# Kernel tuning notes

Measured on AMD Instinct MI355X. Metric: run time of the kernel, lower is better.

## Reference

```python
import jax, jax.numpy as jnp
import numpy as np

NEG_INF = -9e15
ALPHA = 2.0  # LeakyReLU negative slope from init (alpha=2)


def setup_inputs() -> dict:
    key = jax.random.key(0)
    k1, k2, k3, k4 = jax.random.split(key, 4)
    B, N, Fin, Fout = 8, 2048, 256, 128
    x = jax.random.normal(k1, (B, N, Fin), dtype=jnp.float32)
    adj = jax.random.randint(k2, (B, N, N), 0, 2, dtype=jnp.int32)
    # xavier_uniform with gain=1.414
    def xavier(k, shape, gain=1.414):
        fan_in, fan_out = shape[0], shape[1]
        bound = gain * np.sqrt(6.0 / (fan_in + fan_out))
        return jax.random.uniform(k, shape, jnp.float32, -bound, bound)
    W = xavier(k3, (Fin, Fout))
    a = xavier(k4, (2 * Fout, 1))
    return {"x": x, "adj": adj, "W": W, "a": a}


def reference(x, adj, W, a):
    # Wh: [B, N, Fout]
    Wh = jnp.matmul(x, W)
    Fout = W.shape[1]
    a1 = a[:Fout, 0]   # [Fout]
    a2 = a[Fout:, 0]   # [Fout]
    f1 = jnp.einsum('bnf,f->bn', Wh, a1)  # [B, N]
    f2 = jnp.einsum('bnf,f->bn', Wh, a2)  # [B, N]
    e = f1[:, :, None] + f2[:, None, :]   # [B, N, N]
    e = jnp.where(e >= 0, e, ALPHA * e)   # leaky relu, slope 2
    e = jnp.where(adj > 0, e, NEG_INF)
    attention = jax.nn.softmax(e, axis=2)
    # dropout: eval mode (no-op)
    h_prime = jnp.matmul(attention, Wh)   # [B, N, Fout]
    # concat=True -> elu
    return jnp.where(h_prime > 0, h_prime, jnp.expm1(h_prime))
```

## Files before the change

### kernel.cpp

```cpp
#include <hip/hip_runtime.h>
#include <hip/hip_bf16.h>
#include <math.h>

#define NEGINF (-9000000000000000.0f)

constexpr int B_   = 8;
constexpr int N_   = 2048;
constexpr int FIN  = 256;
constexpr int FOUT = 128;
constexpr int TI   = 16;
constexpr int PPAD = 8;
constexpr int PROW = N_ + PPAD;
constexpr int WPAD = 8;
constexpr int WROW = FIN + WPAD;

typedef __attribute__((ext_vector_type(8))) short bf16x8;
typedef __attribute__((ext_vector_type(4))) float f32x4;

static __device__ __forceinline__ unsigned short f2bf(float f) {
    __hip_bfloat16 h = __float2bfloat16(f);
    return *reinterpret_cast<unsigned short*>(&h);
}
static __device__ __forceinline__ float bf2f(unsigned short u) {
    unsigned int v = ((unsigned int)u) << 16;
    return *reinterpret_cast<float*>(&v);
}

__global__ __launch_bounds__(256) void k0_wt(const float* __restrict__ W,
                                             unsigned short* __restrict__ Wt) {
    const int n = blockIdx.x;
    const int k = threadIdx.x;
    Wt[n * FIN + k] = f2bf(W[k * FOUT + n]);
}

__global__ __launch_bounds__(256) void k1_wh(const float* __restrict__ x,
                                             const unsigned short* __restrict__ Wt,
                                             unsigned short* __restrict__ WhT) {
    __shared__ unsigned short wt[FOUT * WROW];
    __shared__ unsigned short xs[64 * WROW];
    const int tid = threadIdx.x;
    const long r0 = (long)blockIdx.x * 64;

    {
        const int4* src = (const int4*)Wt;
        for (int i = tid; i < FOUT * FIN / 8; i += 256) {
            int row = i >> 5;
            int c   = i & 31;
            *(int4*)&wt[row * WROW + c * 8] = src[i];
        }
    }
    {
        const float4* xsrc = (const float4*)(x + r0 * FIN);
        for (int i = tid; i < 64 * FIN / 4; i += 256) {
            float4 v = xsrc[i];
            int row = i >> 6;
            int c   = i & 63;
            ushort4 u;
            u.x = f2bf(v.x); u.y = f2bf(v.y); u.z = f2bf(v.z); u.w = f2bf(v.w);
            *(ushort4*)&xs[row * WROW + c * 4] = u;
        }
    }
    __syncthreads();

    const int wave = tid >> 6, lane = tid & 63;
    const int quad = lane >> 4, l16 = lane & 15;

    f32x4 acc[2][4];
#pragma unroll
    for (int a = 0; a < 2; ++a)
#pragma unroll
        for (int b = 0; b < 4; ++b) acc[a][b] = {0.f, 0.f, 0.f, 0.f};

#pragma unroll
    for (int ks = 0; ks < FIN / 32; ++ks) {
        const int kof = ks * 32 + quad * 8;
        bf16x8 afr[2], bfr[4];
#pragma unroll
        for (int a = 0; a < 2; ++a) {
            const int d = (wave * 2 + a) * 16 + l16;
            afr[a] = *(const bf16x8*)&wt[d * WROW + kof];
        }
#pragma unroll
        for (int b = 0; b < 4; ++b) {
            const int r = b * 16 + l16;
            bfr[b] = *(const bf16x8*)&xs[r * WROW + kof];
        }
#pragma unroll
        for (int a = 0; a < 2; ++a)
#pragma unroll
            for (int b = 0; b < 4; ++b)
                acc[a][b] = __builtin_amdgcn_mfma_f32_16x16x32_bf16(
                    afr[a], bfr[b], acc[a][b], 0, 0, 0);
    }

    const long bb = r0 / N_;
    const long jb = r0 % N_;
    unsigned short* dst = WhT + bb * (long)FOUT * N_;
#pragma unroll
    for (int a = 0; a < 2; ++a)
#pragma unroll
        for (int b = 0; b < 4; ++b) {
            const long j = jb + b * 16 + l16;
#pragma unroll
            for (int r = 0; r < 4; ++r) {
                const int d = (wave * 2 + a) * 16 + quad * 4 + r;
                dst[(long)d * N_ + j] = f2bf(acc[a][b][r]);
            }
        }
}

__global__ __launch_bounds__(256) void k1b_f(const unsigned short* __restrict__ WhT,
                                             const float* __restrict__ a,
                                             float* __restrict__ f1,
                                             float* __restrict__ f2) {
    __shared__ float a1s[FOUT], a2s[FOUT];
    const int tid = threadIdx.x;
    if (tid < FOUT) { a1s[tid] = a[tid]; a2s[tid] = a[FOUT + tid]; }
    __syncthreads();
    const long jflat = (long)blockIdx.x * 256 + tid;
    const long b = jflat / N_, j = jflat % N_;
    const unsigned short* src = WhT + b * (long)FOUT * N_ + j;
    float s1 = 0.f, s2 = 0.f;
#pragma unroll
    for (int d = 0; d < FOUT; ++d) {
        float w = bf2f(src[(long)d * N_]);
        s1 += w * a1s[d];
        s2 += w * a2s[d];
    }
    f1[jflat] = s1;
    f2[jflat] = s2;
}

__global__ __launch_bounds__(256) void k2_attn(const int* __restrict__ adj,
                                               const unsigned short* __restrict__ WhT,
                                               const float* __restrict__ f1,
                                               const float* __restrict__ f2,
                                               float* __restrict__ out) {
    __shared__ unsigned short p[TI * PROW];
    __shared__ float rsum[TI];

    const int tid  = threadIdx.x;
    const int b    = blockIdx.x & 7;
    const int i0   = (blockIdx.x >> 3) * TI;
    const int wave = tid >> 6, lane = tid & 63;
    const int quad = lane >> 4, l16 = lane & 15;

    const float4* f2b4 = (const float4*)(f2 + (size_t)b * N_);

    for (int rr = 0; rr < 4; ++rr) {
        const int ti = wave * 4 + rr;
        const int i  = i0 + ti;
        const float f1i = f1[(size_t)b * N_ + i];
        const int4* arow4 = (const int4*)(adj + ((size_t)b * N_ + i) * (size_t)N_);

        int4   av[8];
        float4 fv[8];
#pragma unroll
        for (int it = 0; it < 8; ++it) {
            av[it] = arow4[lane + it * 64];
            fv[it] = f2b4[lane + it * 64];
        }
        float4 e[8];
        float m = NEGINF;
#pragma unroll
        for (int it = 0; it < 8; ++it) {
            const float4 t = fv[it];
            float e0 = f1i + t.x; e0 = (e0 >= 0.f) ? e0 : 2.f * e0; if (av[it].x <= 0) e0 = NEGINF;
            float e1 = f1i + t.y; e1 = (e1 >= 0.f) ? e1 : 2.f * e1; if (av[it].y <= 0) e1 = NEGINF;
            float e2 = f1i + t.z; e2 = (e2 >= 0.f) ? e2 : 2.f * e2; if (av[it].z <= 0) e2 = NEGINF;
            float e3 = f1i + t.w; e3 = (e3 >= 0.f) ? e3 : 2.f * e3; if (av[it].w <= 0) e3 = NEGINF;
            e[it] = make_float4(e0, e1, e2, e3);
            m = fmaxf(m, fmaxf(fmaxf(e0, e1), fmaxf(e2, e3)));
        }
#pragma unroll
        for (int o = 32; o; o >>= 1) m = fmaxf(m, __shfl_xor(m, o));

        float s = 0.f;
        unsigned short* pr = &p[ti * PROW];
#pragma unroll
        for (int it = 0; it < 8; ++it) {
            const float p0 = __expf(e[it].x - m);
            const float p1 = __expf(e[it].y - m);
            const float p2 = __expf(e[it].z - m);
            const float p3 = __expf(e[it].w - m);
            s += (p0 + p1) + (p2 + p3);
            ushort4 u;
            u.x = f2bf(p0); u.y = f2bf(p1); u.z = f2bf(p2); u.w = f2bf(p3);
            *(ushort4*)&pr[(lane + it * 64) * 4] = u;
        }
#pragma unroll
        for (int o = 32; o; o >>= 1) s += __shfl_xor(s, o);
        if (lane == 0) rsum[ti] = s;
    }
    __syncthreads();

    const int n0 = wave * 32;
    const unsigned short* whb = WhT + (size_t)b * FOUT * N_;
    const unsigned short* pA  = &p[l16 * PROW];
    const unsigned short* wB0 = whb + (size_t)(n0 + l16) * N_;
    const unsigned short* wB1 = whb + (size_t)(n0 + 16 + l16) * N_;

    f32x4 acc0 = {0.f, 0.f, 0.f, 0.f}, acc1 = {0.f, 0.f, 0.f, 0.f};
#pragma unroll 4
    for (int ks = 0; ks < N_ / 32; ++ks) {
        const int kof = ks * 32 + quad * 8;
        bf16x8 afr = *(const bf16x8*)&pA[kof];
        bf16x8 b0  = *(const bf16x8*)&wB0[kof];
        bf16x8 b1  = *(const bf16x8*)&wB1[kof];
        acc0 = __builtin_amdgcn_mfma_f32_16x16x32_bf16(afr, b0, acc0, 0, 0, 0);
        acc1 = __builtin_amdgcn_mfma_f32_16x16x32_bf16(afr, b1, acc1, 0, 0, 0);
    }

#pragma unroll
    for (int r = 0; r < 4; ++r) {
        const int m = quad * 4 + r;
        const float inv = 1.f / rsum[m];
        float v0 = acc0[r] * inv;
        float v1 = acc1[r] * inv;
        v0 = (v0 > 0.f) ? v0 : expm1f(v0);
        v1 = (v1 > 0.f) ? v1 : expm1f(v1);
        const size_t base = ((size_t)b * N_ + i0 + m) * FOUT + n0;
        out[base + l16]      = v0;
        out[base + 16 + l16] = v1;
    }
}

extern "C" void kernel_launch(void* const* d_in, const int* in_sizes, int n_in,
                              void* d_out, int out_size, void* d_ws, size_t ws_size,
                              hipStream_t stream) {
    const float* x   = (const float*)d_in[0];
    const int*   adj = (const int*)d_in[1];
    const float* W   = (const float*)d_in[2];
    const float* a   = (const float*)d_in[3];
    float* out = (float*)d_out;

    unsigned short* WhT = (unsigned short*)d_ws;
    unsigned short* Wt  = WhT + (size_t)B_ * FOUT * N_;
    float* f1 = (float*)(Wt + (size_t)FOUT * FIN);
    float* f2 = f1 + (size_t)B_ * N_;

    hipLaunchKernelGGL(k0_wt, dim3(FOUT), dim3(FIN), 0, stream, W, Wt);
    hipLaunchKernelGGL(k1_wh, dim3(B_ * N_ / 64), dim3(256), 0, stream,
                       x, Wt, WhT);
    hipLaunchKernelGGL(k1b_f, dim3(B_ * N_ / 256), dim3(256), 0, stream,
                       WhT, a, f1, f2);
    hipLaunchKernelGGL(k2_attn, dim3(B_ * N_ / TI), dim3(256), 0, stream,
                       adj, WhT, f1, f2, out);
}
```

Measured before the change: 282.7 us.

## Fuse f1/f2 projection into Wh GEMM and chunk attention with online softmax

The f1/f2 attention projections move into the epilogue of the Wh GEMM. This drops a separate kernel that re-read WhT with strided column access. The Wh GEMM now uses 32-row tiles and reads Wt directly from global memory instead of staging it in shared memory. The attention kernel processes adjacency in 512-column chunks with a running max/sum rescale, shrinking the P buffer in LDS from 16x2048 to 16x512 to improve occupancy. The cost is an extra barrier per chunk and interleaving softmax with MFMA in phases, rather than one long streaming pass.

```diff
diff --git a/kernel.cpp b/kernel.cpp
--- a/kernel.cpp
+++ b/kernel.cpp
@@ -8,11 +8,11 @@
 constexpr int N_   = 2048;
 constexpr int FIN  = 256;
 constexpr int FOUT = 128;
-constexpr int TI   = 16;
-constexpr int PPAD = 8;
-constexpr int PROW = N_ + PPAD;
-constexpr int WPAD = 8;
-constexpr int WROW = FIN + WPAD;
+
+constexpr int CH  = 512;
+constexpr int NCH = N_ / CH;
+constexpr int PR  = CH + 8;
+constexpr int XR  = FIN + 8;
 
 typedef __attribute__((ext_vector_type(8))) short bf16x8;
 typedef __attribute__((ext_vector_type(4))) float f32x4;
@@ -20,10 +20,6 @@
 static __device__ __forceinline__ unsigned short f2bf(float f) {
     __hip_bfloat16 h = __float2bfloat16(f);
     return *reinterpret_cast<unsigned short*>(&h);
-}
-static __device__ __forceinline__ float bf2f(unsigned short u) {
-    unsigned int v = ((unsigned int)u) << 16;
-    return *reinterpret_cast<float*>(&v);
 }
 
 __global__ __launch_bounds__(256) void k0_wt(const float* __restrict__ W,
@@ -33,31 +29,32 @@
     Wt[n * FIN + k] = f2bf(W[k * FOUT + n]);
 }
 
-__global__ __launch_bounds__(256) void k1_wh(const float* __restrict__ x,
+__global__ __launch_bounds__(256) void ka_wh(const float* __restrict__ x,
                                              const unsigned short* __restrict__ Wt,
-                                             unsigned short* __restrict__ WhT) {
-    __shared__ unsigned short wt[FOUT * WROW];
-    __shared__ unsigned short xs[64 * WROW];
+                                             const float* __restrict__ a,
+                                             unsigned short* __restrict__ WhT,
+                                             float* __restrict__ f1,
+                                             float* __restrict__ f2) {
+    __shared__ unsigned short xs[32 * XR];
+    __shared__ float as[2 * FOUT];
+    __shared__ float fred[2][4][32];
+
     const int tid = threadIdx.x;
-    const long r0 = (long)blockIdx.x * 64;
-
+    const int j0  = blockIdx.x * 32;
+    const int b   = j0 >> 11;
+    const int jb  = j0 & (N_ - 1);
+
+    if (tid < 2 * FOUT) as[tid] = a[tid];
     {
-        const int4* src = (const int4*)Wt;
-        for (int i = tid; i < FOUT * FIN / 8; i += 256) {
-            int row = i >> 5;
-            int c   = i & 31;
-            *(int4*)&wt[row * WROW + c * 8] = src[i];
-        }
-    }
-    {
-        const float4* xsrc = (const float4*)(x + r0 * FIN);
-        for (int i = tid; i < 64 * FIN / 4; i += 256) {
-            float4 v = xsrc[i];
-            int row = i >> 6;
-            int c   = i & 63;
+        const float4* xsrc = (const float4*)(x + (size_t)j0 * FIN);
+#pragma unroll
+        for (int t = 0; t < 8; ++t) {
+            const int idx = tid + t * 256;
+            float4 v = xsrc[idx];
+            const int row = idx >> 6, c4 = idx & 63;
             ushort4 u;
             u.x = f2bf(v.x); u.y = f2bf(v.y); u.z = f2bf(v.z); u.w = f2bf(v.w);
-            *(ushort4*)&xs[row * WROW + c * 4] = u;
+            *(ushort4*)&xs[row * XR + c4 * 4] = u;
         }
     }
     __syncthreads();
@@ -65,150 +62,165 @@
     const int wave = tid >> 6, lane = tid & 63;
     const int quad = lane >> 4, l16 = lane & 15;
 
-    f32x4 acc[2][4];
-#pragma unroll
-    for (int a = 0; a < 2; ++a)
-#pragma unroll
-        for (int b = 0; b < 4; ++b) acc[a][b] = {0.f, 0.f, 0.f, 0.f};
-
+    f32x4 acc[2][2];
+#pragma unroll
+    for (int aa = 0; aa < 2; ++aa)
+#pragma unroll
+        for (int nn = 0; nn < 2; ++nn) acc[aa][nn] = {0.f, 0.f, 0.f, 0.f};
+
+    const unsigned short* wtA0 = Wt + (size_t)(32 * wave + l16) * FIN;
+    const unsigned short* wtA1 = wtA0 + 16 * FIN;
 #pragma unroll
     for (int ks = 0; ks < FIN / 32; ++ks) {
         const int kof = ks * 32 + quad * 8;
-        bf16x8 afr[2], bfr[4];
-#pragma unroll
-        for (int a = 0; a < 2; ++a) {
-            const int d = (wave * 2 + a) * 16 + l16;
-            afr[a] = *(const bf16x8*)&wt[d * WROW + kof];
-        }
-#pragma unroll
-        for (int b = 0; b < 4; ++b) {
-            const int r = b * 16 + l16;
-            bfr[b] = *(const bf16x8*)&xs[r * WROW + kof];
-        }
-#pragma unroll
-        for (int a = 0; a < 2; ++a)
-#pragma unroll
-            for (int b = 0; b < 4; ++b)
-                acc[a][b] = __builtin_amdgcn_mfma_f32_16x16x32_bf16(
-                    afr[a], bfr[b], acc[a][b], 0, 0, 0);
-    }
-
-    const long bb = r0 / N_;
-    const long jb = r0 % N_;
-    unsigned short* dst = WhT + bb * (long)FOUT * N_;
-#pragma unroll
-    for (int a = 0; a < 2; ++a)
-#pragma unroll
-        for (int b = 0; b < 4; ++b) {
-            const long j = jb + b * 16 + l16;
+        bf16x8 af0 = *(const bf16x8*)&wtA0[kof];
+        bf16x8 af1 = *(const bf16x8*)&wtA1[kof];
+        bf16x8 bf0 = *(const bf16x8*)&xs[l16 * XR + kof];
+        bf16x8 bf1 = *(const bf16x8*)&xs[(16 + l16) * XR + kof];
+        acc[0][0] = __builtin_amdgcn_mfma_f32_16x16x32_bf16(af0, bf0, acc[0][0], 0, 0, 0);
+        acc[0][1] = __builtin_amdgcn_mfma_f32_16x16x32_bf16(af0, bf1, acc[0][1], 0, 0, 0);
+        acc[1][0] = __builtin_amdgcn_mfma_f32_16x16x32_bf16(af1, bf0, acc[1][0], 0, 0, 0);
+        acc[1][1] = __builtin_amdgcn_mfma_f32_16x16x32_bf16(af1, bf1, acc[1][1], 0, 0, 0);
+    }
+
+    unsigned short* dst = WhT + (size_t)b * FOUT * N_;
+    float pf[2][2] = {{0.f, 0.f}, {0.f, 0.f}};
+#pragma unroll
+    for (int aa = 0; aa < 2; ++aa)
+#pragma unroll
+        for (int nn = 0; nn < 2; ++nn)
 #pragma unroll
             for (int r = 0; r < 4; ++r) {
-                const int d = (wave * 2 + a) * 16 + quad * 4 + r;
-                dst[(long)d * N_ + j] = f2bf(acc[a][b][r]);
+                const int d = 32 * wave + 16 * aa + 4 * quad + r;
+                const int j = jb + 16 * nn + l16;
+                const float v = acc[aa][nn][r];
+                dst[(size_t)d * N_ + j] = f2bf(v);
+                pf[0][nn] += v * as[d];
+                pf[1][nn] += v * as[FOUT + d];
             }
-        }
-}
-
-__global__ __launch_bounds__(256) void k1b_f(const unsigned short* __restrict__ WhT,
-                                             const float* __restrict__ a,
-                                             float* __restrict__ f1,
-                                             float* __restrict__ f2) {
-    __shared__ float a1s[FOUT], a2s[FOUT];
-    const int tid = threadIdx.x;
-    if (tid < FOUT) { a1s[tid] = a[tid]; a2s[tid] = a[FOUT + tid]; }
+#pragma unroll
+    for (int ff = 0; ff < 2; ++ff)
+#pragma unroll
+        for (int nn = 0; nn < 2; ++nn) {
+            float v = pf[ff][nn];
+            v += __shfl_xor(v, 16);
+            v += __shfl_xor(v, 32);
+            pf[ff][nn] = v;
+        }
+    if (quad == 0) {
+#pragma unroll
+        for (int ff = 0; ff < 2; ++ff)
+#pragma unroll
+            for (int nn = 0; nn < 2; ++nn)
+                fred[ff][wave][nn * 16 + l16] = pf[ff][nn];
+    }
     __syncthreads();
-    const long jflat = (long)blockIdx.x * 256 + tid;
-    const long b = jflat / N_, j = jflat % N_;
-    const unsigned short* src = WhT + b * (long)FOUT * N_ + j;
-    float s1 = 0.f, s2 = 0.f;
-#pragma unroll
-    for (int d = 0; d < FOUT; ++d) {
-        float w = bf2f(src[(long)d * N_]);
-        s1 += w * a1s[d];
-        s2 += w * a2s[d];
-    }
-    f1[jflat] = s1;
-    f2[jflat] = s2;
-}
-
-__global__ __launch_bounds__(256) void k2_attn(const int* __restrict__ adj,
+    if (tid < 64) {
+        const int ff = tid >> 5, j32 = tid & 31;
+        const float s = fred[ff][0][j32] + fred[ff][1][j32] +
+                        fred[ff][2][j32] + fred[ff][3][j32];
+        (ff ? f2 : f1)[(size_t)b * N_ + jb + j32] = s;
+    }
+}
+
+__global__ __launch_bounds__(256) void kb_attn(const int* __restrict__ adj,
                                                const unsigned short* __restrict__ WhT,
                                                const float* __restrict__ f1,
                                                const float* __restrict__ f2,
                                                float* __restrict__ out) {
-    __shared__ unsigned short p[TI * PROW];
-    __shared__ float rsum[TI];
+    __shared__ unsigned short p[16 * PR];
+    __shared__ float alpha_s[16];
+    __shared__ float rsum[16];
 
     const int tid  = threadIdx.x;
     const int b    = blockIdx.x & 7;
-    const int i0   = (blockIdx.x >> 3) * TI;
+    const int i0   = (blockIdx.x >> 3) * 16;
     const int wave = tid >> 6, lane = tid & 63;
     const int quad = lane >> 4, l16 = lane & 15;
 
     const float4* f2b4 = (const float4*)(f2 + (size_t)b * N_);
 
-    for (int rr = 0; rr < 4; ++rr) {
-        const int ti = wave * 4 + rr;
-        const int i  = i0 + ti;
-        const float f1i = f1[(size_t)b * N_ + i];
-        const int4* arow4 = (const int4*)(adj + ((size_t)b * N_ + i) * (size_t)N_);
-
-        int4   av[8];
-        float4 fv[8];
-#pragma unroll
-        for (int it = 0; it < 8; ++it) {
-            av[it] = arow4[lane + it * 64];
-            fv[it] = f2b4[lane + it * 64];
-        }
-        float4 e[8];
-        float m = NEGINF;
-#pragma unroll
-        for (int it = 0; it < 8; ++it) {
-            const float4 t = fv[it];
-            float e0 = f1i + t.x; e0 = (e0 >= 0.f) ? e0 : 2.f * e0; if (av[it].x <= 0) e0 = NEGINF;
-            float e1 = f1i + t.y; e1 = (e1 >= 0.f) ? e1 : 2.f * e1; if (av[it].y <= 0) e1 = NEGINF;
-            float e2 = f1i + t.z; e2 = (e2 >= 0.f) ? e2 : 2.f * e2; if (av[it].z <= 0) e2 = NEGINF;
-            float e3 = f1i + t.w; e3 = (e3 >= 0.f) ? e3 : 2.f * e3; if (av[it].w <= 0) e3 = NEGINF;
-            e[it] = make_float4(e0, e1, e2, e3);
-            m = fmaxf(m, fmaxf(fmaxf(e0, e1), fmaxf(e2, e3)));
-        }
-#pragma unroll
-        for (int o = 32; o; o >>= 1) m = fmaxf(m, __shfl_xor(m, o));
-
-        float s = 0.f;
-        unsigned short* pr = &p[ti * PROW];
-#pragma unroll
-        for (int it = 0; it < 8; ++it) {
-            const float p0 = __expf(e[it].x - m);
-            const float p1 = __expf(e[it].y - m);
-            const float p2 = __expf(e[it].z - m);
-            const float p3 = __expf(e[it].w - m);
-            s += (p0 + p1) + (p2 + p3);
-            ushort4 u;
-            u.x = f2bf(p0); u.y = f2bf(p1); u.z = f2bf(p2); u.w = f2bf(p3);
-            *(ushort4*)&pr[(lane + it * 64) * 4] = u;
-        }
-#pragma unroll
-        for (int o = 32; o; o >>= 1) s += __shfl_xor(s, o);
-        if (lane == 0) rsum[ti] = s;
-    }
-    __syncthreads();
-
+    float m_run[4], s_run[4];
+#pragma unroll
+    for (int r = 0; r < 4; ++r) { m_run[r] = NEGINF; s_run[r] = 0.f; }
+
+    f32x4 acc0 = {0.f, 0.f, 0.f, 0.f}, acc1 = {0.f, 0.f, 0.f, 0.f};
     const int n0 = wave * 32;
-    const unsigned short* whb = WhT + (size_t)b * FOUT * N_;
-    const unsigned short* pA  = &p[l16 * PROW];
-    const unsigned short* wB0 = whb + (size_t)(n0 + l16) * N_;
-    const unsigned short* wB1 = whb + (size_t)(n0 + 16 + l16) * N_;
-
-    f32x4 acc0 = {0.f, 0.f, 0.f, 0.f}, acc1 = {0.f, 0.f, 0.f, 0.f};
-#pragma unroll 4
-    for (int ks = 0; ks < N_ / 32; ++ks) {
-        const int kof = ks * 32 + quad * 8;
-        bf16x8 afr = *(const bf16x8*)&pA[kof];
-        bf16x8 b0  = *(const bf16x8*)&wB0[kof];
-        bf16x8 b1  = *(const bf16x8*)&wB1[kof];
-        acc0 = __builtin_amdgcn_mfma_f32_16x16x32_bf16(afr, b0, acc0, 0, 0, 0);
-        acc1 = __builtin_amdgcn_mfma_f32_16x16x32_bf16(afr, b1, acc1, 0, 0, 0);
+    const unsigned short* wB0 = WhT + (size_t)b * FOUT * N_ + (size_t)(n0 + l16) * N_;
+    const unsigned short* wB1 = wB0 + (size_t)16 * N_;
+    const unsigned short* pA  = &p[l16 * PR];
+
+    for (int c = 0; c < NCH; ++c) {
+#pragma unroll
+        for (int rr = 0; rr < 4; ++rr) {
+            const int ti = wave * 4 + rr;
+            const int i  = i0 + ti;
+            const float f1i = f1[(size_t)b * N_ + i];
+            const int4* arow4 = (const int4*)(adj + ((size_t)b * N_ + i) * (size_t)N_);
+            const int c4 = c * (CH / 4);
+            int4   av0 = arow4[c4 + lane];
+            int4   av1 = arow4[c4 + 64 + lane];
+            float4 fv0 = f2b4[c4 + lane];
+            float4 fv1 = f2b4[c4 + 64 + lane];
+
+            float e[8];
+            e[0] = f1i + fv0.x; e[1] = f1i + fv0.y; e[2] = f1i + fv0.z; e[3] = f1i + fv0.w;
+            e[4] = f1i + fv1.x; e[5] = f1i + fv1.y; e[6] = f1i + fv1.z; e[7] = f1i + fv1.w;
+#pragma unroll
+            for (int q = 0; q < 8; ++q) e[q] = (e[q] >= 0.f) ? e[q] : 2.f * e[q];
+            if (av0.x <= 0) e[0] = NEGINF;
+            if (av0.y <= 0) e[1] = NEGINF;
+            if (av0.z <= 0) e[2] = NEGINF;
+            if (av0.w <= 0) e[3] = NEGINF;
+            if (av1.x <= 0) e[4] = NEGINF;
+            if (av1.y <= 0) e[5] = NEGINF;
+            if (av1.z <= 0) e[6] = NEGINF;
+            if (av1.w <= 0) e[7] = NEGINF;
+
+            float mx = e[0];
+#pragma unroll
+            for (int q = 1; q < 8; ++q) mx = fmaxf(mx, e[q]);
+#pragma unroll
+            for (int o = 32; o; o >>= 1) mx = fmaxf(mx, __shfl_xor(mx, o));
+
+            const float mnew = fmaxf(m_run[rr], mx);
+            const float al   = __expf(m_run[rr] - mnew);
+            float pv[8];
+            float s8 = 0.f;
+#pragma unroll
+            for (int q = 0; q < 8; ++q) { pv[q] = __expf(e[q] - mnew); s8 += pv[q]; }
+#pragma unroll
+            for (int o = 32; o; o >>= 1) s8 += __shfl_xor(s8, o);
+            s_run[rr] = s_run[rr] * al + s8;
+            m_run[rr] = mnew;
+
+            ushort4 u0, u1;
+            u0.x = f2bf(pv[0]); u0.y = f2bf(pv[1]); u0.z = f2bf(pv[2]); u0.w = f2bf(pv[3]);
+            u1.x = f2bf(pv[4]); u1.y = f2bf(pv[5]); u1.z = f2bf(pv[6]); u1.w = f2bf(pv[7]);
+            *(ushort4*)&p[ti * PR + 4 * lane]       = u0;
+            *(ushort4*)&p[ti * PR + 256 + 4 * lane] = u1;
+            if (lane == 0) alpha_s[ti] = al;
+            if (c == NCH - 1 && lane == 0) rsum[ti] = s_run[rr];
+        }
+        __syncthreads();
+
+#pragma unroll
+        for (int r = 0; r < 4; ++r) {
+            const float alr = alpha_s[quad * 4 + r];
+            acc0[r] *= alr;
+            acc1[r] *= alr;
+        }
+        const int kbase = c * CH;
+#pragma unroll
+        for (int ks = 0; ks < CH / 32; ++ks) {
+            const int kof = ks * 32 + quad * 8;
+            bf16x8 afr = *(const bf16x8*)&pA[kof];
+            bf16x8 b0  = *(const bf16x8*)&wB0[kbase + kof];
+            bf16x8 b1  = *(const bf16x8*)&wB1[kbase + kof];
+            acc0 = __builtin_amdgcn_mfma_f32_16x16x32_bf16(afr, b0, acc0, 0, 0, 0);
+            acc1 = __builtin_amdgcn_mfma_f32_16x16x32_bf16(afr, b1, acc1, 0, 0, 0);
+        }
+        __syncthreads();
     }
 
 #pragma unroll
@@ -240,10 +252,8 @@
     float* f2 = f1 + (size_t)B_ * N_;
 
     hipLaunchKernelGGL(k0_wt, dim3(FOUT), dim3(FIN), 0, stream, W, Wt);
-    hipLaunchKernelGGL(k1_wh, dim3(B_ * N_ / 64), dim3(256), 0, stream,
-                       x, Wt, WhT);
-    hipLaunchKernelGGL(k1b_f, dim3(B_ * N_ / 256), dim3(256), 0, stream,
-                       WhT, a, f1, f2);
-    hipLaunchKernelGGL(k2_attn, dim3(B_ * N_ / TI), dim3(256), 0, stream,
+    hipLaunchKernelGGL(ka_wh, dim3(B_ * N_ / 32), dim3(256), 0, stream,
+                       x, Wt, a, WhT, f1, f2);
+    hipLaunchKernelGGL(kb_attn, dim3(B_ * N_ / 16), dim3(256), 0, stream,
                        adj, WhT, f1, f2, out);
 }
```

Result: faster. 266.6 us (-5.7%).
